# Kernel optimization log

Hardware: AMD Instinct MI355X
Metric: run time of the kernel (lower is better)

## Reference

```python
import jax, jax.numpy as jnp
import numpy as np

N, E, G = 20000, 320000, 8
H, C = 4, 64
NODE_IN, EDGE_IN, HID = 18, 4, 64
NEG = 0.2    # GATv2 leaky_relu negative slope
EPS = 1e-5   # BatchNorm eps (eval mode: running_mean=0, running_var=1)


def setup_inputs() -> dict:
    key = jax.random.key(0)
    ks = iter(jax.random.split(key, 48))
    rn = lambda shape, s=0.05: jax.random.normal(next(ks), shape, dtype=jnp.float32) * s
    return {
        "x": jax.random.normal(next(ks), (N, NODE_IN), dtype=jnp.float32),
        "edge_attr": jax.random.uniform(next(ks), (E, EDGE_IN), dtype=jnp.float32),
        "enc_w1": rn((NODE_IN, HID)), "enc_b1": jnp.zeros((HID,), jnp.float32),
        "enc_w2": rn((HID, HID)), "enc_b2": jnp.zeros((HID,), jnp.float32),
        "g1_wl": rn((HID, H * C)), "g1_wr": rn((HID, H * C)), "g1_we": rn((EDGE_IN, H * C)),
        "g1_att": rn((H, C)), "g1_b": jnp.zeros((H * C,), jnp.float32),
        "bn1_g": jnp.ones((H * C,), jnp.float32), "bn1_b": jnp.zeros((H * C,), jnp.float32),
        "g2_wl": rn((H * C, H * C)), "g2_wr": rn((H * C, H * C)), "g2_we": rn((EDGE_IN, H * C)),
        "g2_att": rn((H, C)), "g2_b": jnp.zeros((C,), jnp.float32),
        "bn2_g": jnp.ones((C,), jnp.float32), "bn2_b": jnp.zeros((C,), jnp.float32),
        "sage_wl": rn((HID, HID)), "sage_bl": jnp.zeros((HID,), jnp.float32), "sage_wr": rn((HID, HID)),
        "bn3_g": jnp.ones((HID,), jnp.float32), "bn3_b": jnp.zeros((HID,), jnp.float32),
        "gh_w1": rn((2 * HID, HID)), "gh_b1": jnp.zeros((HID,), jnp.float32),
        "gh_w2": rn((HID, 32)), "gh_b2": jnp.zeros((32,), jnp.float32),
        "gh_w3": rn((32, 1)), "gh_b3": jnp.zeros((1,), jnp.float32),
        "eh_w1": rn((2 * HID + EDGE_IN, 32)), "eh_b1": jnp.zeros((32,), jnp.float32),
        "eh_w2": rn((32, 1)), "eh_b2": jnp.zeros((1,), jnp.float32),
        "edge_index": jax.random.randint(next(ks), (2, E), 0, N, dtype=jnp.int32),
        "batch": jnp.sort(jax.random.randint(next(ks), (N,), 0, G, dtype=jnp.int32)),
    }


def _segment_softmax(logits, seg, num):
    mx = jax.ops.segment_max(logits, seg, num_segments=num)
    ex = jnp.exp(logits - mx[seg])
    den = jax.ops.segment_sum(ex, seg, num_segments=num)
    return ex / den[seg]


def _gatv2(h, src, dst, ea, wl, wr, we, att, bias, concat):
    n = h.shape[0]
    xl = (h @ wl).reshape(n, H, C)   # messages come from x_l[src]
    xr = (h @ wr).reshape(n, H, C)
    ee = (ea @ we).reshape(-1, H, C)
    m = xl[src] + xr[dst] + ee                                    # [E', H, C]
    logit = jnp.einsum('ehc,hc->eh', jax.nn.leaky_relu(m, NEG), att)
    alpha = _segment_softmax(logit, dst, n)                       # [E', H]
    out = jax.ops.segment_sum(alpha[:, :, None] * xl[src], dst, num_segments=n)
    if concat:
        return out.reshape(n, H * C) + bias
    return out.mean(axis=1) + bias


def _bn_eval(h, g, b):
    # eval-mode BatchNorm with running_mean=0, running_var=1
    return h * (g / jnp.sqrt(1.0 + EPS)) + b


def reference(x, edge_attr, enc_w1, enc_b1, enc_w2, enc_b2,
              g1_wl, g1_wr, g1_we, g1_att, g1_b, bn1_g, bn1_b,
              g2_wl, g2_wr, g2_we, g2_att, g2_b, bn2_g, bn2_b,
              sage_wl, sage_bl, sage_wr, bn3_g, bn3_b,
              gh_w1, gh_b1, gh_w2, gh_b2, gh_w3, gh_b3,
              eh_w1, eh_b1, eh_w2, eh_b2, edge_index, batch):
    src, dst = edge_index[0], edge_index[1]
    # PyG add_self_loops with fill_value='mean': loop edge_attr = mean of incoming edge_attr
    ones = jnp.ones((E,), jnp.float32)
    cnt = jax.ops.segment_sum(ones, dst, num_segments=N)
    loop_attr = jax.ops.segment_sum(edge_attr, dst, num_segments=N) / jnp.clip(cnt, 1.0)[:, None]
    sl = jnp.arange(N, dtype=src.dtype)
    src_sl = jnp.concatenate([src, sl])
    dst_sl = jnp.concatenate([dst, sl])
    ea_sl = jnp.concatenate([edge_attr, loop_attr], axis=0)

    # ZoneEncoder (dropout inactive in eval)
    h = jax.nn.relu(x @ enc_w1 + enc_b1) @ enc_w2 + enc_b2
    h = _gatv2(h, src_sl, dst_sl, ea_sl, g1_wl, g1_wr, g1_we, g1_att, g1_b, True)
    h = jax.nn.elu(_bn_eval(h, bn1_g, bn1_b))
    h = _gatv2(h, src_sl, dst_sl, ea_sl, g2_wl, g2_wr, g2_we, g2_att, g2_b, False)
    h = jax.nn.elu(_bn_eval(h, bn2_g, bn2_b))
    # SAGEConv: lin_l(mean_{j->i} h_j) + lin_r(h_i), no self loops
    agg = jax.ops.segment_sum(h[src], dst, num_segments=N) / jnp.clip(cnt, 1.0)[:, None]
    h = agg @ sage_wl + sage_bl + h @ sage_wr
    h = jax.nn.relu(_bn_eval(h, bn3_g, bn3_b))
    # global mean + max pooling per graph
    cntg = jax.ops.segment_sum(jnp.ones((N,), jnp.float32), batch, num_segments=G)
    mean_p = jax.ops.segment_sum(h, batch, num_segments=G) / jnp.clip(cntg, 1.0)[:, None]
    max_p = jax.ops.segment_max(h, batch, num_segments=G)
    hp = jnp.concatenate([mean_p, max_p], axis=-1)                # [G, 128]
    z = jax.nn.relu(hp @ gh_w1 + gh_b1)
    z = jax.nn.relu(z @ gh_w2 + gh_b2)
    graph_score = jax.nn.sigmoid(z @ gh_w3 + gh_b3)               # [G, 1]
    ef = jnp.concatenate([h[src], h[dst], edge_attr], axis=-1)    # [E, 132]
    ez = jax.nn.relu(ef @ eh_w1 + eh_b1)
    edge_scores = jax.nn.sigmoid(ez @ eh_w2 + eh_b2)              # [E, 1]
    return (graph_score, edge_scores)
```

## Files before the change

kernel.cpp:

```cpp
#include <hip/hip_runtime.h>

#define NN 20000
#define NE 320000
#define EP (NE + NN)
#define NG 8
#define HC 256
#define NODE_IN 18
#define HID 64
#define NEG_SLOPE 0.2f
#define BN_EPS 1e-5f

#define OFF_XL    0u
#define OFF_XR    5120000u
#define OFF_H1    10240000u
#define OFF_WTL   12800000u
#define OFF_WTR   12832768u
#define OFF_P     13200000u
#define OFF_H2B   13600000u
#define OFF_H0    15360000u
#define OFF_H3    16640000u
#define OFF_ZERO  18000000u
#define OFF_CNT   18000000u
#define OFF_PSUM  18020000u
#define OFF_PMAX  18020512u
#define OFF_PCNT  18021024u
#define ZERO_FLOATS (18021040u - 18000000u)
#define OFF_EACSR 18021040u
#define OFF_RP    19381040u
#define OFF_SRC   19421041u
#define OFF_BSUM  19761056u

#define SCAN_ELEM 1024
#define SCAN_NB ((NN + SCAN_ELEM - 1) / SCAN_ELEM)
#define NB32 (NN / 32)

#define PRE_CNT_NB 1250
#define PRE_CAST_NB 512
#define PRE_ENC_NB 1250
#define POST_EH_NB (NE / 256)
#define POST_POOL_NB ((NN + 255) / 256)

typedef __attribute__((ext_vector_type(8))) short bf16x8_t;
typedef __attribute__((ext_vector_type(4))) float f32x4_t;

__device__ __forceinline__ ushort f2bf(float f) {
  unsigned u = __float_as_uint(f);
  unsigned r = (u + 0x7fffu + ((u >> 16) & 1u)) >> 16;
  return (ushort)r;
}
__device__ __forceinline__ float bf2f(ushort b) {
  return __uint_as_float(((unsigned)b) << 16);
}

#define ENC_NPW 4
__global__ __launch_bounds__(256) void k_pre(
    const int* __restrict__ ei, unsigned* __restrict__ cnt, int* __restrict__ rank,
    const float* __restrict__ Wl, const float* __restrict__ Wr,
    ushort* __restrict__ WtL, ushort* __restrict__ WtR,
    const float* __restrict__ x, const float* __restrict__ ew1, const float* __restrict__ eb1,
    const float* __restrict__ ew2, const float* __restrict__ eb2, float* __restrict__ h0) {
  __shared__ float W1[NODE_IN * HID];
  __shared__ float W2[HID * HID];
  __shared__ float B1s[HID];
  __shared__ float B2s[HID];
  __shared__ float hid_s[4][HID];
  const int b = blockIdx.x;
  const int tid = threadIdx.x;
  if (b < PRE_CNT_NB) {
    int e = b * 256 + tid;
    if (e < NE) {
      int d = ei[NE + e];
      rank[e] = (int)atomicAdd(&cnt[d], 1u);
    }
    return;
  }
  if (b < PRE_CNT_NB + PRE_CAST_NB) {
    int bb = b - PRE_CNT_NB;
    const float* W = (bb < 256) ? Wl : Wr;
    ushort* Wt = (bb < 256) ? WtL : WtR;
    int k = bb & 255;
    Wt[tid * 256 + k] = f2bf(W[k * 256 + tid]);
    return;
  }
  const int eb = b - PRE_CNT_NB - PRE_CAST_NB;
  for (int i = tid; i < NODE_IN * HID; i += 256) W1[i] = ew1[i];
  for (int i = tid; i < HID * HID; i += 256) W2[i] = ew2[i];
  if (tid < HID) { B1s[tid] = eb1[tid]; B2s[tid] = eb2[tid]; }
  __syncthreads();
  const int lane = tid & 63;
  const int w = tid >> 6;
  #pragma unroll
  for (int t = 0; t < ENC_NPW; t++) {
    const int n = eb * (4 * ENC_NPW) + w * ENC_NPW + t;
    const float* xp = &x[(size_t)n * NODE_IN];
    float s = B1s[lane];
    #pragma unroll
    for (int i = 0; i < NODE_IN; i++) s += xp[i] * W1[i * HID + lane];
    hid_s[w][lane] = fmaxf(s, 0.f);
    float o = B2s[lane];
    #pragma unroll 8
    for (int k = 0; k < HID; k++) o += hid_s[w][k] * W2[k * HID + lane];
    h0[(size_t)n * HID + lane] = o;
  }
}

__global__ __launch_bounds__(256) void k_scan_blk(
    const unsigned* __restrict__ cnt, int* __restrict__ row_ptr, int* __restrict__ bsums) {
  __shared__ int wsum[4];
  const int tid = threadIdx.x, lane = tid & 63, w = tid >> 6;
  const int i0 = blockIdx.x * SCAN_ELEM + tid * 4;
  int v0 = (i0 + 0 < NN) ? ((int)cnt[i0 + 0] + 1) : 0;
  int v1 = (i0 + 1 < NN) ? ((int)cnt[i0 + 1] + 1) : 0;
  int v2 = (i0 + 2 < NN) ? ((int)cnt[i0 + 2] + 1) : 0;
  int v3 = (i0 + 3 < NN) ? ((int)cnt[i0 + 3] + 1) : 0;
  int tsum = v0 + v1 + v2 + v3;
  int incl = tsum;
  #pragma unroll
  for (int off = 1; off < 64; off <<= 1) {
    int t = __shfl_up(incl, off);
    if (lane >= off) incl += t;
  }
  if (lane == 63) wsum[w] = incl;
  __syncthreads();
  int p = incl - tsum;
  #pragma unroll
  for (int k = 0; k < 4; k++) if (k < w) p += wsum[k];
  if (i0 + 0 < NN) row_ptr[i0 + 0] = p;
  if (i0 + 1 < NN) row_ptr[i0 + 1] = p + v0;
  if (i0 + 2 < NN) row_ptr[i0 + 2] = p + v0 + v1;
  if (i0 + 3 < NN) row_ptr[i0 + 3] = p + v0 + v1 + v2;
  if (tid == 0) bsums[blockIdx.x] = wsum[0] + wsum[1] + wsum[2] + wsum[3];
}

__global__ __launch_bounds__(256) void k_scan_add(
    const int* __restrict__ bsums, int* __restrict__ row_ptr) {
  const int b = blockIdx.x, tid = threadIdx.x;
  int off = 0;
  for (int j = 0; j < b; j++) off += bsums[j];
  const int i0 = b * SCAN_ELEM + tid * 4;
  #pragma unroll
  for (int k = 0; k < 4; k++) {
    int i = i0 + k;
    if (i < NN) row_ptr[i] += off;
  }
  if (b == 0 && tid == 0) row_ptr[NN] = EP;
}

__global__ __launch_bounds__(256) void k_csr_scatter(
    const int* __restrict__ ei, const int* __restrict__ rank,
    const int* __restrict__ row_ptr, const float* __restrict__ ea,
    int* __restrict__ srcs, float* __restrict__ ea_csr) {
  int e = blockIdx.x * 256 + threadIdx.x;
  if (e >= NE) return;
  int s = ei[e], d = ei[NE + e];
  int p = row_ptr[d] + rank[e];
  srcs[p] = s;
  *(float4*)&ea_csr[(size_t)p * 4] = *(const float4*)&ea[(size_t)e * 4];
}

__global__ __launch_bounds__(256) void k_loop_row(
    const int* __restrict__ row_ptr, int* __restrict__ srcs, float* __restrict__ ea_csr) {
  int lane = threadIdx.x & 63, w = threadIdx.x >> 6;
  int i = blockIdx.x * 4 + w;
  int start = row_ptr[i], last = row_ptr[i + 1] - 1;
  float s = 0.f;
  int base = start * 4;
  int nfl = (last - start) * 4;
  for (int f = lane; f < nfl; f += 64) s += ea_csr[base + f];
  s += __shfl_xor(s, 4);
  s += __shfl_xor(s, 8);
  s += __shfl_xor(s, 16);
  s += __shfl_xor(s, 32);
  float c = (float)(last - start);
  if (c < 1.f) c = 1.f;
  if (lane < 4) ea_csr[(size_t)last * 4 + lane] = s / c;
  if (lane == 0) srcs[last] = i | (int)0x80000000;
}

__global__ __launch_bounds__(256) void k_gemm256_dual(
    const float* __restrict__ A, const float* __restrict__ Wl_, const float* __restrict__ Wr_,
    ushort* __restrict__ OUTbf, float* __restrict__ OUTf) {
  const bool first = blockIdx.x < NB32;
  const float* __restrict__ W = first ? Wl_ : Wr_;
  const int n0 = (first ? blockIdx.x : blockIdx.x - NB32) * 32;
  __shared__ float Wlds[32 * 256];
  __shared__ float Al[32 * 36];
  const int tid = threadIdx.x;
  const int tx = tid & 63, ty = tid >> 6;
  float acc[8][4];
  #pragma unroll
  for (int m = 0; m < 8; m++)
    #pragma unroll
    for (int c = 0; c < 4; c++) acc[m][c] = 0.f;

  for (int kt = 0; kt < 64; kt += 32) {
    #pragma unroll
    for (int r = 0; r < 8; r++) {
      int i4 = tid + 256 * r;
      int row = i4 >> 6;
      int col4 = (i4 & 63) * 4;
      *(float4*)&Wlds[row * 256 + col4] = *(const float4*)&W[(size_t)(kt + row) * 256 + col4];
    }
    {
      int m = tid >> 3, kk = (tid & 7) * 4;
      float4 av = *(const float4*)&A[(size_t)(n0 + m) * 64 + kt + kk];
      Al[(kk + 0) * 36 + m] = av.x;
      Al[(kk + 1) * 36 + m] = av.y;
      Al[(kk + 2) * 36 + m] = av.z;
      Al[(kk + 3) * 36 + m] = av.w;
    }
    __syncthreads();
    #pragma unroll 8
    for (int k = 0; k < 32; k++) {
      float4 b = *(float4*)&Wlds[k * 256 + tx * 4];
      float4 a0v = *(float4*)&Al[k * 36 + ty * 8];
      float4 a1v = *(float4*)&Al[k * 36 + ty * 8 + 4];
      float am[8] = {a0v.x, a0v.y, a0v.z, a0v.w, a1v.x, a1v.y, a1v.z, a1v.w};
      #pragma unroll
      for (int m = 0; m < 8; m++) {
        acc[m][0] += am[m] * b.x;
        acc[m][1] += am[m] * b.y;
        acc[m][2] += am[m] * b.z;
        acc[m][3] += am[m] * b.w;
      }
    }
    __syncthreads();
  }
  if (first) {
    #pragma unroll
    for (int m = 0; m < 8; m++) {
      ushort4 o = {f2bf(acc[m][0]), f2bf(acc[m][1]), f2bf(acc[m][2]), f2bf(acc[m][3])};
      *(ushort4*)&OUTbf[(size_t)(n0 + ty * 8 + m) * 256 + tx * 4] = o;
    }
  } else {
    #pragma unroll
    for (int m = 0; m < 8; m++) {
      float4 o = {acc[m][0], acc[m][1], acc[m][2], acc[m][3]};
      *(float4*)&OUTf[(size_t)(n0 + ty * 8 + m) * 256 + tx * 4] = o;
    }
  }
}

__global__ __launch_bounds__(256) void k_gemm_mfma_dual(
    const ushort* __restrict__ A, const ushort* __restrict__ wtl,
    const ushort* __restrict__ wtr, ushort* __restrict__ OUTbf, float* __restrict__ OUTf) {
  const bool first = blockIdx.x < NB32;
  const ushort* __restrict__ Wt = first ? wtl : wtr;
  const int n0 = (first ? blockIdx.x : blockIdx.x - NB32) * 32;
  __shared__ ushort Asub[32][72];
  __shared__ ushort Wsub[256][72];
  const int tid = threadIdx.x;
  const int lane = tid & 63;
  const int w = tid >> 6;
  const int lr = lane & 15;
  const int lk = (lane >> 4) * 8;

  f32x4_t acc[2][4];
  #pragma unroll
  for (int m = 0; m < 2; m++)
    #pragma unroll
    for (int n = 0; n < 4; n++) acc[m][n] = (f32x4_t){0.f, 0.f, 0.f, 0.f};

  for (int kt = 0; kt < 256; kt += 64) {
    {
      int r = tid >> 3, seg = (tid & 7) * 8;
      *(uint4*)&Asub[r][seg] = *(const uint4*)&A[(size_t)(n0 + r) * 256 + kt + seg];
    }
    #pragma unroll
    for (int rep = 0; rep < 8; rep++) {
      int idx = rep * 256 + tid;
      int r = idx >> 3, seg = (idx & 7) * 8;
      *(uint4*)&Wsub[r][seg] = *(const uint4*)&Wt[(size_t)r * 256 + kt + seg];
    }
    __syncthreads();
    #pragma unroll
    for (int kk = 0; kk < 2; kk++) {
      bf16x8_t af0 = *(bf16x8_t*)&Asub[lr][kk * 32 + lk];
      bf16x8_t af1 = *(bf16x8_t*)&Asub[16 + lr][kk * 32 + lk];
      #pragma unroll
      for (int n = 0; n < 4; n++) {
        bf16x8_t bfr = *(bf16x8_t*)&Wsub[w * 64 + n * 16 + lr][kk * 32 + lk];
        acc[0][n] = __builtin_amdgcn_mfma_f32_16x16x32_bf16(af0, bfr, acc[0][n], 0, 0, 0);
        acc[1][n] = __builtin_amdgcn_mfma_f32_16x16x32_bf16(af1, bfr, acc[1][n], 0, 0, 0);
      }
    }
    __syncthreads();
  }
  const int crow = (lane >> 4) * 4;
  #pragma unroll
  for (int m = 0; m < 2; m++) {
    #pragma unroll
    for (int n = 0; n < 4; n++) {
      int col = w * 64 + n * 16 + lr;
      #pragma unroll
      for (int r = 0; r < 4; r++) {
        int row = n0 + m * 16 + crow + r;
        if (first) OUTbf[(size_t)row * 256 + col] = f2bf(acc[m][n][r]);
        else       OUTf[(size_t)row * 256 + col] = acc[m][n][r];
      }
    }
  }
}

#define GAT_EDGE(A_, U_, DN_, C0_, C1_, C2_, C3_)                                  \
  {                                                                                \
    float xx_ = bf2f((U_).x), xy_ = bf2f((U_).y), xz_ = bf2f((U_).z), xw_ = bf2f((U_).w); \
    float m0_ = xx_ + xrd.x + (A_).x * we0.x + (A_).y * we1.x + (A_).z * we2.x + (A_).w * we3.x; \
    float m1_ = xy_ + xrd.y + (A_).x * we0.y + (A_).y * we1.y + (A_).z * we2.y + (A_).w * we3.y; \
    float m2_ = xz_ + xrd.z + (A_).x * we0.z + (A_).y * we1.z + (A_).z * we2.z + (A_).w * we3.z; \
    float m3_ = xw_ + xrd.w + (A_).x * we0.w + (A_).y * we1.w + (A_).z * we2.w + (A_).w * we3.w; \
    m0_ = fmaxf(m0_, NEG_SLOPE * m0_);                                             \
    m1_ = fmaxf(m1_, NEG_SLOPE * m1_);                                             \
    m2_ = fmaxf(m2_, NEG_SLOPE * m2_);                                             \
    m3_ = fmaxf(m3_, NEG_SLOPE * m3_);                                             \
    float lg_ = m0_ * attv.x + m1_ * attv.y + m2_ * attv.z + m3_ * attv.w;         \
    lg_ += __shfl_xor(lg_, 1);                                                     \
    lg_ += __shfl_xor(lg_, 2);                                                     \
    lg_ += __shfl_xor(lg_, 4);                                                     \
    lg_ += __shfl_xor(lg_, 8);                                                     \
    float p_ = __expf(lg_);                                                        \
    DN_ += p_;                                                                     \
    C0_ = fmaf(p_, xx_, C0_);                                                      \
    C1_ = fmaf(p_, xy_, C1_);                                                      \
    C2_ = fmaf(p_, xz_, C2_);                                                      \
    C3_ = fmaf(p_, xw_, C3_);                                                      \
  }

template <int CONCAT>
__global__ __launch_bounds__(256) void k_gat_fused(
    const ushort* __restrict__ xl, const float* __restrict__ xr,
    const float* __restrict__ we, const float* __restrict__ att,
    const int* __restrict__ srcs, const float* __restrict__ ea_csr,
    const int* __restrict__ row_ptr,
    const float* __restrict__ bias, const float* __restrict__ bng,
    const float* __restrict__ bnb, void* __restrict__ outp,
    ushort* __restrict__ outbf2) {
  const int lane = threadIdx.x & 63;
  const int w = threadIdx.x >> 6;
  const int i = blockIdx.x * 4 + w;
  const int c0 = lane * 4;

  const float4 attv = *(const float4*)&att[c0];
  const float4 we0 = *(const float4*)&we[0 * HC + c0];
  const float4 we1 = *(const float4*)&we[1 * HC + c0];
  const float4 we2 = *(const float4*)&we[2 * HC + c0];
  const float4 we3 = *(const float4*)&we[3 * HC + c0];
  const float4 xrd = *(const float4*)&xr[(size_t)i * HC + c0];

  const int start = row_ptr[i];
  const int deg = row_ptr[i + 1] - start;

  float dnA = 0.f, aA0 = 0.f, aA1 = 0.f, aA2 = 0.f, aA3 = 0.f;
  float dnB = 0.f, aB0 = 0.f, aB1 = 0.f, aB2 = 0.f, aB3 = 0.f;
  float dnC = 0.f, aC0 = 0.f, aC1 = 0.f, aC2 = 0.f, aC3 = 0.f;
  float dnD = 0.f, aD0 = 0.f, aD1 = 0.f, aD2 = 0.f, aD3 = 0.f;

  for (int base = 0; base < deg; base += 64) {
    int rem = deg - base;
    if (rem > 64) rem = 64;
    int sv = 0;
    if (lane < rem) sv = srcs[start + base + lane] & 0x7fffffff;
    const float4* eaB = (const float4*)&ea_csr[(size_t)(start + base) * 4];
    int jj = 0;
    for (; jj + 4 <= rem; jj += 4) {
      int s0 = __shfl(sv, jj);
      int s1 = __shfl(sv, jj + 1);
      int s2 = __shfl(sv, jj + 2);
      int s3 = __shfl(sv, jj + 3);
      float4 a0 = eaB[jj];
      float4 a1 = eaB[jj + 1];
      float4 a2 = eaB[jj + 2];
      float4 a3 = eaB[jj + 3];
      ushort4 u0 = *(const ushort4*)&xl[(size_t)s0 * HC + c0];
      ushort4 u1 = *(const ushort4*)&xl[(size_t)s1 * HC + c0];
      ushort4 u2 = *(const ushort4*)&xl[(size_t)s2 * HC + c0];
      ushort4 u3 = *(const ushort4*)&xl[(size_t)s3 * HC + c0];
      GAT_EDGE(a0, u0, dnA, aA0, aA1, aA2, aA3);
      GAT_EDGE(a1, u1, dnB, aB0, aB1, aB2, aB3);
      GAT_EDGE(a2, u2, dnC, aC0, aC1, aC2, aC3);
      GAT_EDGE(a3, u3, dnD, aD0, aD1, aD2, aD3);
    }
    for (; jj < rem; ++jj) {
      int s0 = __shfl(sv, jj);
      float4 a0 = eaB[jj];
      ushort4 u0 = *(const ushort4*)&xl[(size_t)s0 * HC + c0];
      GAT_EDGE(a0, u0, dnA, aA0, aA1, aA2, aA3);
    }
  }

  float rinv = 1.f / ((dnA + dnB) + (dnC + dnD));
  float acc0 = ((aA0 + aB0) + (aC0 + aD0)) * rinv;
  float acc1 = ((aA1 + aB1) + (aC1 + aD1)) * rinv;
  float acc2 = ((aA2 + aB2) + (aC2 + aD2)) * rinv;
  float acc3 = ((aA3 + aB3) + (aC3 + aD3)) * rinv;

  const float inv_sqrt = rsqrtf(1.f + BN_EPS);
  if (CONCAT) {
    float4 bi = *(const float4*)&bias[c0];
    float4 g = *(const float4*)&bng[c0];
    float4 bb = *(const float4*)&bnb[c0];
    float v0 = (acc0 + bi.x) * (g.x * inv_sqrt) + bb.x;
    float v1 = (acc1 + bi.y) * (g.y * inv_sqrt) + bb.y;
    float v2 = (acc2 + bi.z) * (g.z * inv_sqrt) + bb.z;
    float v3 = (acc3 + bi.w) * (g.w * inv_sqrt) + bb.w;
    v0 = (v0 > 0.f) ? v0 : (__expf(v0) - 1.f);
    v1 = (v1 > 0.f) ? v1 : (__expf(v1) - 1.f);
    v2 = (v2 > 0.f) ? v2 : (__expf(v2) - 1.f);
    v3 = (v3 > 0.f) ? v3 : (__expf(v3) - 1.f);
    ushort* op = (ushort*)outp;
    ushort4 o = {f2bf(v0), f2bf(v1), f2bf(v2), f2bf(v3)};
    *(ushort4*)&op[(size_t)i * HC + c0] = o;
  } else {
    acc0 += __shfl_xor(acc0, 16); acc0 += __shfl_xor(acc0, 32);
    acc1 += __shfl_xor(acc1, 16); acc1 += __shfl_xor(acc1, 32);
    acc2 += __shfl_xor(acc2, 16); acc2 += __shfl_xor(acc2, 32);
    acc3 += __shfl_xor(acc3, 16); acc3 += __shfl_xor(acc3, 32);
    if (lane < 16) {
      int cc = lane * 4;
      float4 bi = *(const float4*)&bias[cc];
      float4 g = *(const float4*)&bng[cc];
      float4 bb = *(const float4*)&bnb[cc];
      float v0 = (0.25f * acc0 + bi.x) * (g.x * inv_sqrt) + bb.x;
      float v1 = (0.25f * acc1 + bi.y) * (g.y * inv_sqrt) + bb.y;
      float v2 = (0.25f * acc2 + bi.z) * (g.z * inv_sqrt) + bb.z;
      float v3 = (0.25f * acc3 + bi.w) * (g.w * inv_sqrt) + bb.w;
      v0 = (v0 > 0.f) ? v0 : (__expf(v0) - 1.f);
      v1 = (v1 > 0.f) ? v1 : (__expf(v1) - 1.f);
      v2 = (v2 > 0.f) ? v2 : (__expf(v2) - 1.f);
      v3 = (v3 > 0.f) ? v3 : (__expf(v3) - 1.f);
      float* op = (float*)outp;
      float4 o = {v0, v1, v2, v3};
      *(float4*)&op[(size_t)i * 64 + cc] = o;
      ushort4 ob = {f2bf(v0), f2bf(v1), f2bf(v2), f2bf(v3)};
      *(ushort4*)&outbf2[(size_t)i * 64 + cc] = ob;
    }
  }
}

__global__ __launch_bounds__(256) void k_sage(
    const float* __restrict__ h2, const ushort* __restrict__ h2b,
    const int* __restrict__ row_ptr,
    const int* __restrict__ srcs, const unsigned* __restrict__ cnt,
    const float* __restrict__ wl, const float* __restrict__ bl,
    const float* __restrict__ wr, const float* __restrict__ bng,
    const float* __restrict__ bnb, const float* __restrict__ w1eh,
    float* __restrict__ h3, ushort* __restrict__ P) {
  __shared__ float Wc[64][64];
  __shared__ float agg_s[4][64];
  __shared__ float h2_s[4][64];
  int tid = threadIdx.x;
  for (int idx = tid; idx < 4096; idx += 256) {
    int k = idx >> 6, j = idx & 63;
    Wc[k][j] = (j < 32) ? w1eh[k * 32 + j] : w1eh[(64 + k) * 32 + (j - 32)];
  }
  int lane = tid & 63;
  int w = tid >> 6;
  int i = blockIdx.x * 4 + w;
  int start = row_ptr[i];
  int nreal = row_ptr[i + 1] - 1 - start;
  float a0 = 0.f, a1 = 0.f, a2 = 0.f, a3 = 0.f;
  for (int base = 0; base < nreal; base += 64) {
    int rem = nreal - base;
    if (rem > 64) rem = 64;
    int sv = 0;
    if (lane < rem) sv = srcs[start + base + lane];
    int jj = 0;
    for (; jj + 4 <= rem; jj += 4) {
      int s0 = __shfl(sv, jj);
      int s1 = __shfl(sv, jj + 1);
      int s2 = __shfl(sv, jj + 2);
      int s3 = __shfl(sv, jj + 3);
      a0 += bf2f(h2b[(size_t)s0 * 64 + lane]);
      a1 += bf2f(h2b[(size_t)s1 * 64 + lane]);
      a2 += bf2f(h2b[(size_t)s2 * 64 + lane]);
      a3 += bf2f(h2b[(size_t)s3 * 64 + lane]);
    }
    for (; jj < rem; ++jj) {
      int s0 = __shfl(sv, jj);
      a0 += bf2f(h2b[(size_t)s0 * 64 + lane]);
    }
  }
  float a = (a0 + a1) + (a2 + a3);
  float c = (float)cnt[i];
  if (c < 1.f) c = 1.f;
  agg_s[w][lane] = a / c;
  h2_s[w][lane] = h2[(size_t)i * 64 + lane];
  __syncthreads();
  float s = bl[lane];
  #pragma unroll 4
  for (int k = 0; k < 64; k++)
    s += agg_s[w][k] * wl[k * 64 + lane] + h2_s[w][k] * wr[k * 64 + lane];
  s = s * (bng[lane] * rsqrtf(1.f + BN_EPS)) + bnb[lane];
  s = fmaxf(s, 0.f);
  h3[(size_t)i * 64 + lane] = s;
  agg_s[w][lane] = s;
  float p = 0.f;
  #pragma unroll 4
  for (int k = 0; k < 64; k++) p += agg_s[w][k] * Wc[k][lane];
  P[(size_t)i * 64 + lane] = f2bf(p);
}

__global__ __launch_bounds__(256) void k_post(
    const ushort* __restrict__ P, const int* __restrict__ ei,
    const float* __restrict__ ea, const float* __restrict__ w1eh,
    const float* __restrict__ b1, const float* __restrict__ w2,
    const float* __restrict__ b2, float* __restrict__ out,
    const float* __restrict__ h3, const int* __restrict__ batch,
    float* __restrict__ psum, float* __restrict__ pmax, float* __restrict__ pcnt) {
  const int tid = threadIdx.x;
  if (blockIdx.x >= POST_EH_NB) {
    int pb = blockIdx.x - POST_EH_NB;
    int j = tid & 63, grp = tid >> 6;
    int nbase = pb * 256 + grp * 64;
    float s = 0.f, m = 0.f, cn = 0.f;
    int cur = -1;
    for (int t = 0; t < 64; t++) {
      int n = nbase + t;
      if (n >= NN) break;
      int g = batch[n];
      if (g != cur) {
        if (cur >= 0) {
          atomicAdd(&psum[cur * 64 + j], s);
          atomicMax((int*)&pmax[cur * 64 + j], __float_as_int(m));
          if (j == 0) atomicAdd(&pcnt[cur], cn);
        }
        cur = g; s = 0.f; m = 0.f; cn = 0.f;
      }
      float v = h3[(size_t)n * 64 + j];
      s += v; m = fmaxf(m, v); cn += 1.f;
    }
    if (cur >= 0) {
      atomicAdd(&psum[cur * 64 + j], s);
      atomicMax((int*)&pmax[cur * 64 + j], __float_as_int(m));
      if (j == 0) atomicAdd(&pcnt[cur], cn);
    }
    return;
  }
  const int e = blockIdx.x * 256 + tid;
  const int sn = ei[e], dn = ei[NE + e];
  const ushort* Ps = &P[(size_t)sn * 64];
  const ushort* Pd = &P[(size_t)dn * 64 + 32];
  float acc[32];
  #pragma unroll
  for (int f = 0; f < 4; f++) {
    ushort u1[8], u2[8];
    *(uint4*)u1 = *(const uint4*)&Ps[f * 8];
    *(uint4*)u2 = *(const uint4*)&Pd[f * 8];
    #pragma unroll
    for (int j = 0; j < 8; j++) acc[f * 8 + j] = bf2f(u1[j]) + bf2f(u2[j]);
  }
  float4 av = *(const float4*)&ea[(size_t)e * 4];
  const float* w1c = &w1eh[128 * 32];
  float z = 0.f;
  #pragma unroll
  for (int j = 0; j < 32; j++) {
    float v = acc[j] + b1[j]
            + av.x * w1c[j] + av.y * w1c[32 + j]
            + av.z * w1c[64 + j] + av.w * w1c[96 + j];
    z += fmaxf(v, 0.f) * w2[j];
  }
  out[e] = 1.f / (1.f + __expf(-(z + b2[0])));
}

__global__ void k_graph_head(
    const float* __restrict__ psum, const float* __restrict__ pmax,
    const float* __restrict__ pcnt,
    const float* __restrict__ w1, const float* __restrict__ b1,
    const float* __restrict__ w2, const float* __restrict__ b2,
    const float* __restrict__ w3, const float* __restrict__ b3,
    float* __restrict__ out) {
  __shared__ float hp[128];
  __shared__ float z1[64];
  __shared__ float z2[32];
  int g = blockIdx.x, j = threadIdx.x;
  float c = pcnt[g];
  if (c < 1.f) c = 1.f;
  hp[j] = psum[g * 64 + j] / c;
  hp[64 + j] = pmax[g * 64 + j];
  __syncthreads();
  float s = b1[j];
  #pragma unroll 8
  for (int k = 0; k < 128; k++) s += hp[k] * w1[k * 64 + j];
  z1[j] = fmaxf(s, 0.f);
  __syncthreads();
  if (j < 32) {
    float s2 = b2[j];
    #pragma unroll 8
    for (int k = 0; k < 64; k++) s2 += z1[k] * w2[k * 32 + j];
    z2[j] = fmaxf(s2, 0.f);
  }
  __syncthreads();
  if (j == 0) {
    float s3 = b3[0];
    #pragma unroll
    for (int k = 0; k < 32; k++) s3 += z2[k] * w3[k];
    out[g] = 1.f / (1.f + expf(-s3));
  }
}

extern "C" void kernel_launch(void* const* d_in, const int* in_sizes, int n_in,
                              void* d_out, int out_size, void* d_ws, size_t ws_size,
                              hipStream_t stream) {
  const float* x         = (const float*)d_in[0];
  const float* edge_attr = (const float*)d_in[1];
  const float* enc_w1 = (const float*)d_in[2];
  const float* enc_b1 = (const float*)d_in[3];
  const float* enc_w2 = (const float*)d_in[4];
  const float* enc_b2 = (const float*)d_in[5];
  const float* g1_wl = (const float*)d_in[6];
  const float* g1_wr = (const float*)d_in[7];
  const float* g1_we = (const float*)d_in[8];
  const float* g1_att = (const float*)d_in[9];
  const float* g1_b = (const float*)d_in[10];
  const float* bn1_g = (const float*)d_in[11];
  const float* bn1_b = (const float*)d_in[12];
  const float* g2_wl = (const float*)d_in[13];
  const float* g2_wr = (const float*)d_in[14];
  const float* g2_we = (const float*)d_in[15];
  const float* g2_att = (const float*)d_in[16];
  const float* g2_b = (const float*)d_in[17];
  const float* bn2_g = (const float*)d_in[18];
  const float* bn2_b = (const float*)d_in[19];
  const float* sage_wl = (const float*)d_in[20];
  const float* sage_bl = (const float*)d_in[21];
  const float* sage_wr = (const float*)d_in[22];
  const float* bn3_g = (const float*)d_in[23];
  const float* bn3_b = (const float*)d_in[24];
  const float* gh_w1 = (const float*)d_in[25];
  const float* gh_b1 = (const float*)d_in[26];
  const float* gh_w2 = (const float*)d_in[27];
  const float* gh_b2 = (const float*)d_in[28];
  const float* gh_w3 = (const float*)d_in[29];
  const float* gh_b3 = (const float*)d_in[30];
  const float* eh_w1 = (const float*)d_in[31];
  const float* eh_b1 = (const float*)d_in[32];
  const float* eh_w2 = (const float*)d_in[33];
  const float* eh_b2 = (const float*)d_in[34];
  const int* ei    = (const int*)d_in[35];
  const int* batch = (const int*)d_in[36];
  float* out = (float*)d_out;

  float* ws = (float*)d_ws;
  ushort* xlbf = (ushort*)(ws + OFF_XL);
  float* xr = ws + OFF_XR;
  ushort* h1bf = (ushort*)(ws + OFF_H1);
  ushort* wtl = (ushort*)(ws + OFF_WTL);
  ushort* wtr = (ushort*)(ws + OFF_WTR);
  ushort* Pproj = (ushort*)(ws + OFF_P);
  ushort* h2b = (ushort*)(ws + OFF_H2B);
  float* h0 = ws + OFF_H0;
  float* h3 = ws + OFF_H3;
  unsigned* cnt = (unsigned*)(ws + OFF_CNT);
  float* psum = ws + OFF_PSUM;
  float* pmax = ws + OFF_PMAX;
  float* pcnt = ws + OFF_PCNT;
  float* ea_csr = ws + OFF_EACSR;
  int* row_ptr = (int*)(ws + OFF_RP);
  int* srcs = (int*)(ws + OFF_SRC);
  int* bsums = (int*)(ws + OFF_BSUM);
  int* rank = (int*)(ws + OFF_XL);

  hipMemsetAsync(ws + OFF_ZERO, 0, ZERO_FLOATS * sizeof(float), stream);

  k_pre<<<PRE_CNT_NB + PRE_CAST_NB + PRE_ENC_NB, 256, 0, stream>>>(
      ei, cnt, rank, g2_wl, g2_wr, wtl, wtr,
      x, enc_w1, enc_b1, enc_w2, enc_b2, h0);
  k_scan_blk<<<SCAN_NB, 256, 0, stream>>>(cnt, row_ptr, bsums);
  k_scan_add<<<SCAN_NB, 256, 0, stream>>>(bsums, row_ptr);
  k_csr_scatter<<<NE / 256, 256, 0, stream>>>(ei, rank, row_ptr, edge_attr, srcs, ea_csr);
  k_loop_row<<<NN / 4, 256, 0, stream>>>(row_ptr, srcs, ea_csr);

  k_gemm256_dual<<<2 * NB32, 256, 0, stream>>>(h0, g1_wl, g1_wr, xlbf, xr);
  k_gat_fused<1><<<NN / 4, 256, 0, stream>>>(xlbf, xr, g1_we, g1_att, srcs, ea_csr,
                                             row_ptr, g1_b, bn1_g, bn1_b, (void*)h1bf, nullptr);

  k_gemm_mfma_dual<<<2 * NB32, 256, 0, stream>>>(h1bf, wtl, wtr, xlbf, xr);
  k_gat_fused<0><<<NN / 4, 256, 0, stream>>>(xlbf, xr, g2_we, g2_att, srcs, ea_csr,
                                             row_ptr, g2_b, bn2_g, bn2_b, (void*)h0, h2b);

  k_sage<<<NN / 4, 256, 0, stream>>>(h0, h2b, row_ptr, srcs, cnt, sage_wl, sage_bl, sage_wr,
                                     bn3_g, bn3_b, eh_w1, h3, Pproj);

  k_post<<<POST_EH_NB + POST_POOL_NB, 256, 0, stream>>>(
      Pproj, ei, edge_attr, eh_w1, eh_b1, eh_w2, eh_b2, out + NG,
      h3, batch, psum, pmax, pcnt);
  k_graph_head<<<NG, 64, 0, stream>>>(psum, pmax, pcnt, gh_w1, gh_b1, gh_w2, gh_b2, gh_w3, gh_b3, out);
}
```

Before: 306.0 us.

## Bucket nodes by in-degree so each block processes similar-degree rows

Adds a counting-sort pass (bucket count, scan, permutation) that orders nodes by in-degree, and makes the GAT and SAGE kernels map each wave to a node through this permutation. The goal is to balance work within a block so the four waves finish together, reducing idle time caused by degree imbalance. In exchange it adds three small kernels plus a memset, and it scatters per-node reads and writes (xr, outputs, row_ptr) to non-contiguous addresses. The workspace offsets for P and H2B are moved to make room for the new arrays.

```diff
diff --git a/kernel.cpp b/kernel.cpp
--- a/kernel.cpp
+++ b/kernel.cpp
@@ -15,8 +15,12 @@
 #define OFF_H1    10240000u
 #define OFF_WTL   12800000u
 #define OFF_WTR   12832768u
-#define OFF_P     13200000u
-#define OFF_H2B   13600000u
+#define OFF_P     13000000u
+#define OFF_H2B   13700000u
+#define OFF_PERM  14400000u
+#define OFF_ORD   14450000u
+#define OFF_BCNT  14500000u
+#define OFF_BB    14510000u
 #define OFF_H0    15360000u
 #define OFF_H3    16640000u
 #define OFF_ZERO  18000000u
@@ -144,6 +148,39 @@
     if (i < NN) row_ptr[i] += off;
   }
   if (b == 0 && tid == 0) row_ptr[NN] = EP;
+}
+
+__global__ __launch_bounds__(256) void k_bucket(
+    const unsigned* __restrict__ cnt, int* __restrict__ bcnt, int* __restrict__ ord) {
+  int i = blockIdx.x * 256 + threadIdx.x;
+  if (i >= NN) return;
+  int d = (int)cnt[i];
+  if (d > 255) d = 255;
+  ord[i] = atomicAdd(&bcnt[d], 1);
+}
+
+__global__ void k_bscan(const int* __restrict__ bcnt, int* __restrict__ bb) {
+  __shared__ int lds[256];
+  int tid = threadIdx.x;
+  lds[tid] = bcnt[tid];
+  __syncthreads();
+  for (int off = 1; off < 256; off <<= 1) {
+    int t = (tid >= off) ? lds[tid - off] : 0;
+    __syncthreads();
+    lds[tid] += t;
+    __syncthreads();
+  }
+  bb[tid] = lds[tid] - bcnt[tid];
+}
+
+__global__ __launch_bounds__(256) void k_perm(
+    const unsigned* __restrict__ cnt, const int* __restrict__ ord,
+    const int* __restrict__ bb, int* __restrict__ perm) {
+  int i = blockIdx.x * 256 + threadIdx.x;
+  if (i >= NN) return;
+  int d = (int)cnt[i];
+  if (d > 255) d = 255;
+  perm[bb[d] + ord[i]] = i;
 }
 
 __global__ __launch_bounds__(256) void k_csr_scatter(
@@ -331,13 +368,13 @@
     const ushort* __restrict__ xl, const float* __restrict__ xr,
     const float* __restrict__ we, const float* __restrict__ att,
     const int* __restrict__ srcs, const float* __restrict__ ea_csr,
-    const int* __restrict__ row_ptr,
+    const int* __restrict__ row_ptr, const int* __restrict__ perm,
     const float* __restrict__ bias, const float* __restrict__ bng,
     const float* __restrict__ bnb, void* __restrict__ outp,
     ushort* __restrict__ outbf2) {
   const int lane = threadIdx.x & 63;
   const int w = threadIdx.x >> 6;
-  const int i = blockIdx.x * 4 + w;
+  const int i = perm[blockIdx.x * 4 + w];
   const int c0 = lane * 4;
 
   const float4 attv = *(const float4*)&att[c0];
@@ -439,7 +476,7 @@
 
 __global__ __launch_bounds__(256) void k_sage(
     const float* __restrict__ h2, const ushort* __restrict__ h2b,
-    const int* __restrict__ row_ptr,
+    const int* __restrict__ row_ptr, const int* __restrict__ perm,
     const int* __restrict__ srcs, const unsigned* __restrict__ cnt,
     const float* __restrict__ wl, const float* __restrict__ bl,
     const float* __restrict__ wr, const float* __restrict__ bng,
@@ -455,7 +492,7 @@
   }
   int lane = tid & 63;
   int w = tid >> 6;
-  int i = blockIdx.x * 4 + w;
+  int i = perm[blockIdx.x * 4 + w];
   int start = row_ptr[i];
   int nreal = row_ptr[i + 1] - 1 - start;
   float a0 = 0.f, a1 = 0.f, a2 = 0.f, a3 = 0.f;
@@ -648,6 +685,10 @@
   ushort* wtr = (ushort*)(ws + OFF_WTR);
   ushort* Pproj = (ushort*)(ws + OFF_P);
   ushort* h2b = (ushort*)(ws + OFF_H2B);
+  int* perm = (int*)(ws + OFF_PERM);
+  int* ord = (int*)(ws + OFF_ORD);
+  int* bcnt = (int*)(ws + OFF_BCNT);
+  int* bb = (int*)(ws + OFF_BB);
   float* h0 = ws + OFF_H0;
   float* h3 = ws + OFF_H3;
   unsigned* cnt = (unsigned*)(ws + OFF_CNT);
@@ -661,24 +702,28 @@
   int* rank = (int*)(ws + OFF_XL);
 
   hipMemsetAsync(ws + OFF_ZERO, 0, ZERO_FLOATS * sizeof(float), stream);
+  hipMemsetAsync(ws + OFF_BCNT, 0, 256 * sizeof(int), stream);
 
   k_pre<<<PRE_CNT_NB + PRE_CAST_NB + PRE_ENC_NB, 256, 0, stream>>>(
       ei, cnt, rank, g2_wl, g2_wr, wtl, wtr,
       x, enc_w1, enc_b1, enc_w2, enc_b2, h0);
   k_scan_blk<<<SCAN_NB, 256, 0, stream>>>(cnt, row_ptr, bsums);
   k_scan_add<<<SCAN_NB, 256, 0, stream>>>(bsums, row_ptr);
+  k_bucket<<<(NN + 255) / 256, 256, 0, stream>>>(cnt, bcnt, ord);
+  k_bscan<<<1, 256, 0, stream>>>(bcnt, bb);
+  k_perm<<<(NN + 255) / 256, 256, 0, stream>>>(cnt, ord, bb, perm);
   k_csr_scatter<<<NE / 256, 256, 0, stream>>>(ei, rank, row_ptr, edge_attr, srcs, ea_csr);
   k_loop_row<<<NN / 4, 256, 0, stream>>>(row_ptr, srcs, ea_csr);
 
   k_gemm256_dual<<<2 * NB32, 256, 0, stream>>>(h0, g1_wl, g1_wr, xlbf, xr);
   k_gat_fused<1><<<NN / 4, 256, 0, stream>>>(xlbf, xr, g1_we, g1_att, srcs, ea_csr,
-                                             row_ptr, g1_b, bn1_g, bn1_b, (void*)h1bf, nullptr);
+                                             row_ptr, perm, g1_b, bn1_g, bn1_b, (void*)h1bf, nullptr);
 
   k_gemm_mfma_dual<<<2 * NB32, 256, 0, stream>>>(h1bf, wtl, wtr, xlbf, xr);
   k_gat_fused<0><<<NN / 4, 256, 0, stream>>>(xlbf, xr, g2_we, g2_att, srcs, ea_csr,
-                                             row_ptr, g2_b, bn2_g, bn2_b, (void*)h0, h2b);
-
-  k_sage<<<NN / 4, 256, 0, stream>>>(h0, h2b, row_ptr, srcs, cnt, sage_wl, sage_bl, sage_wr,
+                                             row_ptr, perm, g2_b, bn2_g, bn2_b, (void*)h0, h2b);
+
+  k_sage<<<NN / 4, 256, 0, stream>>>(h0, h2b, row_ptr, perm, srcs, cnt, sage_wl, sage_bl, sage_wr,
                                      bn3_g, bn3_b, eh_w1, h3, Pproj);
 
   k_post<<<POST_EH_NB + POST_POOL_NB, 256, 0, stream>>>(
```

Measured after the change: 361.5 us. +18.2%, slower.
